# Performance work log

Hardware: AMD Instinct MI355X
Metric: run time of the kernel (lower is better)

## Reference

```python
import jax, jax.numpy as jnp
import numpy as np

SEQ_LEN, BATCH, HID, ATT = 2048, 64, 512, 512


def setup_inputs() -> dict:
    key = jax.random.key(0)
    k1, k2, k3, k4, k5, k6 = jax.random.split(key, 6)
    return {
        "dec_out": jax.random.normal(k1, (BATCH, HID), dtype=jnp.float32),
        "enc_outs": jax.random.normal(k2, (SEQ_LEN, BATCH, HID), dtype=jnp.float32),
        "W_s": jax.random.normal(k3, (ATT, HID), dtype=jnp.float32) * (1.0 / np.sqrt(HID)),
        "W_t": jax.random.normal(k4, (ATT, HID), dtype=jnp.float32) * (1.0 / np.sqrt(HID)),
        "b_t": jax.random.normal(k5, (ATT,), dtype=jnp.float32) * 0.01,
        "v_a": jax.random.uniform(k6, (ATT,), dtype=jnp.float32, minval=-0.05, maxval=0.05),
    }


def reference(dec_out, enc_outs, W_s, W_t, b_t, v_a):
    # enc_att: (seq_len, batch, att) = W_s @ enc_outs
    enc_att = jnp.einsum('sbh,ah->sba', enc_outs, W_s)
    # dec_att: (batch, att) = W_t @ dec_out + b_t
    dec_att = dec_out @ W_t.T + b_t
    # score(b, s) = v_a . tanh(enc_att[s,b] + dec_att[b])
    scores = jnp.einsum('sba,a->bs', jnp.tanh(enc_att + dec_att[None, :, :]), v_a)
    return scores  # (batch, seq_len)
```

## Files before the change

### kernel.cpp

```cpp
#include <hip/hip_runtime.h>

typedef __attribute__((ext_vector_type(8))) short short8;
typedef __attribute__((ext_vector_type(4))) float f32x4;

#define SEQ 2048
#define BATCH 64
#define HID 512
#define ATT 512
#define SPB 8
#define DPF 2

__device__ __forceinline__ unsigned short f2bf(float f) {
  unsigned u = __float_as_uint(f);
  u += 0x7fffu + ((u >> 16) & 1u);
  return (unsigned short)(u >> 16);
}
__device__ __forceinline__ float bf2f(unsigned short h) {
  return __uint_as_float(((unsigned)h) << 16);
}

__global__ void bahdanau_pre(const float* __restrict__ dec_out,
                             const float* __restrict__ W_t,
                             const float* __restrict__ b_t,
                             const float* __restrict__ W_s,
                             unsigned short* __restrict__ wsb,
                             float* __restrict__ dec_att) {
  if (blockIdx.x < 64) {
    const int b = blockIdx.x;
    __shared__ float drow[HID];
    for (int i = threadIdx.x; i < HID; i += 256) drow[i] = dec_out[b * HID + i];
    __syncthreads();
    for (int a = threadIdx.x; a < ATT; a += 256) {
      const float4* wr = (const float4*)(W_t + (size_t)a * HID);
      float s0 = 0.f, s1 = 0.f, s2 = 0.f, s3 = 0.f;
#pragma unroll 4
      for (int j = 0; j < HID / 4; ++j) {
        float4 w = wr[j];
        s0 = fmaf(w.x, drow[4 * j + 0], s0);
        s1 = fmaf(w.y, drow[4 * j + 1], s1);
        s2 = fmaf(w.z, drow[4 * j + 2], s2);
        s3 = fmaf(w.w, drow[4 * j + 3], s3);
      }
      dec_att[b * ATT + a] = (s0 + s1) + (s2 + s3) + b_t[a];
    }
  } else {
    const int cb = blockIdx.x - 64;
    const float4* src = (const float4*)W_s;
#pragma unroll
    for (int i = 0; i < 4; ++i) {
      int idx = cb * 1024 + i * 256 + threadIdx.x;
      float4 v = src[idx];
      ushort4 o;
      o.x = f2bf(v.x); o.y = f2bf(v.y); o.z = f2bf(v.z); o.w = f2bf(v.w);
      ((ushort4*)wsb)[idx] = o;
    }
  }
}

__global__ __launch_bounds__(512, 2)
void bahdanau_main(const float* __restrict__ enc,
                   const unsigned short* __restrict__ wsb,
                   const float* __restrict__ dec_att,
                   const float* __restrict__ v_a,
                   float* __restrict__ out) {
  __shared__ __align__(16) unsigned short Albuf[64 * 65 * 8];
  __shared__ __align__(16) unsigned short decl[64 * 520];
  __shared__ float partial[512];

  const int tid  = threadIdx.x;
  const int wave = tid >> 6;
  const int lane = tid & 63;
  const int c = lane & 15;
  const int q = lane >> 4;
  const int n0 = wave * 64;
  const int s0 = blockIdx.x * SPB;

  {
    const float4* dsrc = (const float4*)dec_att;
#pragma unroll
    for (int i = 0; i < 16; ++i) {
      int idx = i * 512 + tid;
      float4 v = dsrc[idx];
      int e = idx * 4;
      int row = e >> 9, col = e & 511;
      ushort4 o;
      o.x = f2bf(v.x); o.y = f2bf(v.y); o.z = f2bf(v.z); o.w = f2bf(v.w);
      *(ushort4*)&decl[row * 520 + col] = o;
    }
  }

  const int srow = tid >> 3;
  const int skc  = (tid & 7) * 4;
  const int ldst = (((skc >> 3) & 3) * 65 + srow) * 8 + (skc & 7);
  const float* gbase = enc + ((size_t)s0 * 64 + srow) * HID + skc;

  float4 stg[16];
#pragma unroll
  for (int kk = 0; kk < 16; ++kk) stg[kk] = *(const float4*)(gbase + kk * 32);

  const unsigned short* bsrc = wsb + (size_t)(n0 + c) * HID + q * 8;

  float va[4];
#pragma unroll
  for (int nt = 0; nt < 4; ++nt) va[nt] = v_a[n0 + nt * 16 + c];

  for (int si = 0; si < SPB; ++si) {
    __syncthreads();

    if (si > 0 && tid < 64) {
      float sum = 0.f;
#pragma unroll
      for (int w = 0; w < 8; ++w) sum += partial[w * 64 + tid];
      out[(size_t)tid * SEQ + (s0 + si - 1)] = sum;
    }

#pragma unroll
    for (int kk = 0; kk < 16; ++kk) {
      ushort4 o;
      o.x = f2bf(stg[kk].x); o.y = f2bf(stg[kk].y);
      o.z = f2bf(stg[kk].z); o.w = f2bf(stg[kk].w);
      *(ushort4*)&Albuf[kk * 2080 + ldst] = o;
    }

    __syncthreads();

    const float* gnext = gbase + (size_t)(si + 1) * (64 * HID);
    const bool more = (si + 1 < SPB);

    short8 bp[DPF][4];
#pragma unroll
    for (int d = 0; d < DPF; ++d)
#pragma unroll
      for (int nt = 0; nt < 4; ++nt)
        bp[d][nt] = *(const short8*)(bsrc + (size_t)nt * 16 * HID + d * 32);

    f32x4 acc[4][4] = {};

#pragma unroll
    for (int kk = 0; kk < 16; ++kk) {
      const unsigned short* ab = &Albuf[kk * 2080 + (q * 65 + c) * 8];
      short8 a4[4];
#pragma unroll
      for (int mt = 0; mt < 4; ++mt)
        a4[mt] = *(const short8*)(ab + mt * 16 * 8);

#pragma unroll
      for (int mt = 0; mt < 4; ++mt)
#pragma unroll
        for (int nt = 0; nt < 4; ++nt)
          acc[mt][nt] = __builtin_amdgcn_mfma_f32_16x16x32_bf16(a4[mt], bp[kk % DPF][nt], acc[mt][nt], 0, 0, 0);

      if (kk + DPF < 16) {
#pragma unroll
        for (int nt = 0; nt < 4; ++nt)
          bp[kk % DPF][nt] = *(const short8*)(bsrc + (size_t)nt * 16 * HID + (kk + DPF) * 32);
      }
      if (more) stg[kk] = *(const float4*)(gnext + kk * 32);
    }

    float rowsum[4][4];
#pragma unroll
    for (int mt = 0; mt < 4; ++mt) {
#pragma unroll
      for (int r = 0; r < 4; ++r) {
        const int ml = mt * 16 + q * 4 + r;
        float sum = 0.f;
#pragma unroll
        for (int nt = 0; nt < 4; ++nt) {
          const int n = n0 + nt * 16 + c;
          float x = acc[mt][nt][r] + bf2f(decl[ml * 520 + n]);
          float e = __builtin_amdgcn_exp2f(x * 2.8853900817779268f);
          float t = 1.f - 2.f * __builtin_amdgcn_rcpf(e + 1.f);
          sum = fmaf(va[nt], t, sum);
        }
        rowsum[mt][r] = sum;
      }
    }

#pragma unroll
    for (int off = 1; off < 16; off <<= 1) {
#pragma unroll
      for (int mt = 0; mt < 4; ++mt)
#pragma unroll
        for (int r = 0; r < 4; ++r)
          rowsum[mt][r] += __shfl_xor(rowsum[mt][r], off, 64);
    }

    if (c == 0) {
#pragma unroll
      for (int mt = 0; mt < 4; ++mt)
#pragma unroll
        for (int r = 0; r < 4; ++r)
          partial[wave * 64 + mt * 16 + q * 4 + r] = rowsum[mt][r];
    }
  }

  __syncthreads();
  if (tid < 64) {
    float sum = 0.f;
#pragma unroll
    for (int w = 0; w < 8; ++w) sum += partial[w * 64 + tid];
    out[(size_t)tid * SEQ + (s0 + SPB - 1)] = sum;
  }
}

extern "C" void kernel_launch(void* const* d_in, const int* in_sizes, int n_in,
                              void* d_out, int out_size, void* d_ws, size_t ws_size,
                              hipStream_t stream) {
  const float* dec_out = (const float*)d_in[0];
  const float* enc     = (const float*)d_in[1];
  const float* W_s     = (const float*)d_in[2];
  const float* W_t     = (const float*)d_in[3];
  const float* b_t     = (const float*)d_in[4];
  const float* v_a     = (const float*)d_in[5];
  float* out = (float*)d_out;

  unsigned short* wsb = (unsigned short*)d_ws;
  float* dec_att = (float*)((char*)d_ws + (size_t)ATT * HID * 2);

  bahdanau_pre<<<128, 256, 0, stream>>>(dec_out, W_t, b_t, W_s, wsb, dec_att);
  bahdanau_main<<<SEQ / SPB, 512, 0, stream>>>(enc, wsb, dec_att, v_a, out);
}
```

Measured before the change: 542.5 us.

## Double-buffer A tile in LDS, init accumulators from transposed dec_att, cut staging registers

Stores dec_att transposed in fp32 and loads it straight into the MFMA accumulators as their initial value. This removes the bf16 LDS copy of dec_att and the per-element add in the epilogue. The encoder tile is now double-buffered in LDS, and the next step's tile is converted and written during the current MFMA loop through a 4-entry register stage instead of 16. That drops one barrier per step and lowers register pressure, at the cost of a larger LDS footprint. The B-operand prefetch reads two slices past the end of the row on the last iterations; those values are never used.

```diff
diff --git a/kernel.cpp b/kernel.cpp
--- a/kernel.cpp
+++ b/kernel.cpp
@@ -8,15 +8,11 @@
 #define HID 512
 #define ATT 512
 #define SPB 8
-#define DPF 2
 
 __device__ __forceinline__ unsigned short f2bf(float f) {
   unsigned u = __float_as_uint(f);
   u += 0x7fffu + ((u >> 16) & 1u);
   return (unsigned short)(u >> 16);
-}
-__device__ __forceinline__ float bf2f(unsigned short h) {
-  return __uint_as_float(((unsigned)h) << 16);
 }
 
 __global__ void bahdanau_pre(const float* __restrict__ dec_out,
@@ -24,7 +20,7 @@
                              const float* __restrict__ b_t,
                              const float* __restrict__ W_s,
                              unsigned short* __restrict__ wsb,
-                             float* __restrict__ dec_att) {
+                             float* __restrict__ decT) {
   if (blockIdx.x < 64) {
     const int b = blockIdx.x;
     __shared__ float drow[HID];
@@ -41,7 +37,7 @@
         s2 = fmaf(w.z, drow[4 * j + 2], s2);
         s3 = fmaf(w.w, drow[4 * j + 3], s3);
       }
-      dec_att[b * ATT + a] = (s0 + s1) + (s2 + s3) + b_t[a];
+      decT[a * BATCH + b] = (s0 + s1) + (s2 + s3) + b_t[a];
     }
   } else {
     const int cb = blockIdx.x - 64;
@@ -60,12 +56,11 @@
 __global__ __launch_bounds__(512, 2)
 void bahdanau_main(const float* __restrict__ enc,
                    const unsigned short* __restrict__ wsb,
-                   const float* __restrict__ dec_att,
+                   const float* __restrict__ decT,
                    const float* __restrict__ v_a,
                    float* __restrict__ out) {
-  __shared__ __align__(16) unsigned short Albuf[64 * 65 * 8];
-  __shared__ __align__(16) unsigned short decl[64 * 520];
-  __shared__ float partial[512];
+  __shared__ __align__(16) unsigned short Albuf[2][16 * 4 * 65 * 8];
+  __shared__ float partial[2][512];
 
   const int tid  = threadIdx.x;
   const int wave = tid >> 6;
@@ -75,87 +70,88 @@
   const int n0 = wave * 64;
   const int s0 = blockIdx.x * SPB;
 
-  {
-    const float4* dsrc = (const float4*)dec_att;
-#pragma unroll
-    for (int i = 0; i < 16; ++i) {
-      int idx = i * 512 + tid;
-      float4 v = dsrc[idx];
-      int e = idx * 4;
-      int row = e >> 9, col = e & 511;
-      ushort4 o;
-      o.x = f2bf(v.x); o.y = f2bf(v.y); o.z = f2bf(v.z); o.w = f2bf(v.w);
-      *(ushort4*)&decl[row * 520 + col] = o;
-    }
-  }
-
   const int srow = tid >> 3;
   const int skc  = (tid & 7) * 4;
   const int ldst = (((skc >> 3) & 3) * 65 + srow) * 8 + (skc & 7);
   const float* gbase = enc + ((size_t)s0 * 64 + srow) * HID + skc;
 
-  float4 stg[16];
-#pragma unroll
-  for (int kk = 0; kk < 16; ++kk) stg[kk] = *(const float4*)(gbase + kk * 32);
-
   const unsigned short* bsrc = wsb + (size_t)(n0 + c) * HID + q * 8;
 
   float va[4];
 #pragma unroll
   for (int nt = 0; nt < 4; ++nt) va[nt] = v_a[n0 + nt * 16 + c];
 
+#pragma unroll 1
+  for (int g = 0; g < 4; ++g) {
+    float4 v[4];
+#pragma unroll
+    for (int u = 0; u < 4; ++u) v[u] = *(const float4*)(gbase + (g * 4 + u) * 32);
+#pragma unroll
+    for (int u = 0; u < 4; ++u) {
+      ushort4 o;
+      o.x = f2bf(v[u].x); o.y = f2bf(v[u].y); o.z = f2bf(v[u].z); o.w = f2bf(v[u].w);
+      *(ushort4*)&Albuf[0][(g * 4 + u) * 2080 + ldst] = o;
+    }
+  }
+  __syncthreads();
+
+#pragma unroll 1
   for (int si = 0; si < SPB; ++si) {
-    __syncthreads();
-
-    if (si > 0 && tid < 64) {
-      float sum = 0.f;
-#pragma unroll
-      for (int w = 0; w < 8; ++w) sum += partial[w * 64 + tid];
-      out[(size_t)tid * SEQ + (s0 + si - 1)] = sum;
-    }
-
-#pragma unroll
-    for (int kk = 0; kk < 16; ++kk) {
-      ushort4 o;
-      o.x = f2bf(stg[kk].x); o.y = f2bf(stg[kk].y);
-      o.z = f2bf(stg[kk].z); o.w = f2bf(stg[kk].w);
-      *(ushort4*)&Albuf[kk * 2080 + ldst] = o;
-    }
-
-    __syncthreads();
-
+    unsigned short* Acur = Albuf[si & 1];
+    unsigned short* Anxt = Albuf[(si & 1) ^ 1];
+    const bool more = (si + 1 < SPB);
     const float* gnext = gbase + (size_t)(si + 1) * (64 * HID);
-    const bool more = (si + 1 < SPB);
-
-    short8 bp[DPF][4];
-#pragma unroll
-    for (int d = 0; d < DPF; ++d)
+
+    f32x4 acc[4][4];
+#pragma unroll
+    for (int nt = 0; nt < 4; ++nt)
+#pragma unroll
+      for (int mt = 0; mt < 4; ++mt)
+        acc[mt][nt] = *(const f32x4*)(decT + (size_t)(n0 + nt * 16 + c) * 64 + mt * 16 + q * 4);
+
+    short8 bp[2][4];
+#pragma unroll
+    for (int d = 0; d < 2; ++d)
 #pragma unroll
       for (int nt = 0; nt < 4; ++nt)
-        bp[d][nt] = *(const short8*)(bsrc + (size_t)nt * 16 * HID + d * 32);
-
-    f32x4 acc[4][4] = {};
-
-#pragma unroll
-    for (int kk = 0; kk < 16; ++kk) {
-      const unsigned short* ab = &Albuf[kk * 2080 + (q * 65 + c) * 8];
-      short8 a4[4];
-#pragma unroll
-      for (int mt = 0; mt < 4; ++mt)
-        a4[mt] = *(const short8*)(ab + mt * 16 * 8);
-
-#pragma unroll
-      for (int mt = 0; mt < 4; ++mt)
+        bp[d][nt] = *(const short8*)(bsrc + nt * 16 * HID + d * 32);
+
+    float4 stg[4];
+    if (more) {
+#pragma unroll
+      for (int u = 0; u < 4; ++u) stg[u] = *(const float4*)(gnext + u * 32);
+    }
+
+#pragma unroll 1
+    for (int g = 0; g < 4; ++g) {
+#pragma unroll
+      for (int u = 0; u < 4; ++u) {
+        const int kk = g * 4 + u;
+
+        const unsigned short* ab = &Acur[kk * 2080 + (q * 65 + c) * 8];
+        short8 a4[4];
+#pragma unroll
+        for (int mt = 0; mt < 4; ++mt)
+          a4[mt] = *(const short8*)(ab + mt * 128);
+
+#pragma unroll
+        for (int mt = 0; mt < 4; ++mt)
+#pragma unroll
+          for (int nt = 0; nt < 4; ++nt)
+            acc[mt][nt] = __builtin_amdgcn_mfma_f32_16x16x32_bf16(a4[mt], bp[u & 1][nt], acc[mt][nt], 0, 0, 0);
+
 #pragma unroll
         for (int nt = 0; nt < 4; ++nt)
-          acc[mt][nt] = __builtin_amdgcn_mfma_f32_16x16x32_bf16(a4[mt], bp[kk % DPF][nt], acc[mt][nt], 0, 0, 0);
-
-      if (kk + DPF < 16) {
-#pragma unroll
-        for (int nt = 0; nt < 4; ++nt)
-          bp[kk % DPF][nt] = *(const short8*)(bsrc + (size_t)nt * 16 * HID + (kk + DPF) * 32);
+          bp[u & 1][nt] = *(const short8*)(bsrc + nt * 16 * HID + (kk + 2) * 32);
+
+        if (more) {
+          ushort4 o;
+          o.x = f2bf(stg[u].x); o.y = f2bf(stg[u].y);
+          o.z = f2bf(stg[u].z); o.w = f2bf(stg[u].w);
+          *(ushort4*)&Anxt[kk * 2080 + ldst] = o;
+          if (kk < 12) stg[u] = *(const float4*)(gnext + (kk + 4) * 32);
+        }
       }
-      if (more) stg[kk] = *(const float4*)(gnext + kk * 32);
     }
 
     float rowsum[4][4];
@@ -163,12 +159,10 @@
     for (int mt = 0; mt < 4; ++mt) {
 #pragma unroll
       for (int r = 0; r < 4; ++r) {
-        const int ml = mt * 16 + q * 4 + r;
         float sum = 0.f;
 #pragma unroll
         for (int nt = 0; nt < 4; ++nt) {
-          const int n = n0 + nt * 16 + c;
-          float x = acc[mt][nt][r] + bf2f(decl[ml * 520 + n]);
+          float x = acc[mt][nt][r];
           float e = __builtin_amdgcn_exp2f(x * 2.8853900817779268f);
           float t = 1.f - 2.f * __builtin_amdgcn_rcpf(e + 1.f);
           sum = fmaf(va[nt], t, sum);
@@ -191,16 +185,17 @@
       for (int mt = 0; mt < 4; ++mt)
 #pragma unroll
         for (int r = 0; r < 4; ++r)
-          partial[wave * 64 + mt * 16 + q * 4 + r] = rowsum[mt][r];
-    }
-  }
-
-  __syncthreads();
-  if (tid < 64) {
-    float sum = 0.f;
-#pragma unroll
-    for (int w = 0; w < 8; ++w) sum += partial[w * 64 + tid];
-    out[(size_t)tid * SEQ + (s0 + SPB - 1)] = sum;
+          partial[si & 1][wave * 64 + mt * 16 + q * 4 + r] = rowsum[mt][r];
+    }
+
+    __syncthreads();
+
+    if (tid < 64) {
+      float sum = 0.f;
+#pragma unroll
+      for (int w = 0; w < 8; ++w) sum += partial[si & 1][w * 64 + tid];
+      out[(size_t)tid * SEQ + s0 + si] = sum;
+    }
   }
 }
 
@@ -216,8 +211,8 @@
   float* out = (float*)d_out;
 
   unsigned short* wsb = (unsigned short*)d_ws;
-  float* dec_att = (float*)((char*)d_ws + (size_t)ATT * HID * 2);
-
-  bahdanau_pre<<<128, 256, 0, stream>>>(dec_out, W_t, b_t, W_s, wsb, dec_att);
-  bahdanau_main<<<SEQ / SPB, 512, 0, stream>>>(enc, wsb, dec_att, v_a, out);
-}
+  float* decT = (float*)((char*)d_ws + (size_t)ATT * HID * 2);
+
+  bahdanau_pre<<<128, 256, 0, stream>>>(dec_out, W_t, b_t, W_s, wsb, decT);
+  bahdanau_main<<<SEQ / SPB, 512, 0, stream>>>(enc, wsb, decT, v_a, out);
+}
```

New measurement: 523.6 us. 3.5% less time.
